# Performance work log

Measured on AMD Instinct MI355X. Metric: run time of the kernel, lower is better.

Reference implementation:

```python
import jax, jax.numpy as jnp
import numpy as np

N = 200000          # number of nodes (V)
NNZ = N * 32        # sparse adjacency non-zeros (avg degree 32)
D_IN, D_HID, N_CLASS = 128, 16, 40  # h = [nfeat, 2**(l+2), nclass] for l=2


def setup_inputs() -> dict:
    key = jax.random.key(0)
    ks = jax.random.split(key, 8)
    H = jax.random.normal(ks[0], (N, D_IN), dtype=jnp.float32)
    rows = jax.random.randint(ks[1], (NNZ,), 0, N)
    cols = jax.random.randint(ks[2], (NNZ,), 0, N)
    # symnormalised adjacency values are positive floats in (0,1]
    vals = jax.random.uniform(ks[3], (NNZ,), dtype=jnp.float32)
    std1 = 1.0 / np.sqrt(D_HID)
    W1 = jax.random.uniform(ks[4], (D_IN, D_HID), jnp.float32, -std1, std1)
    b1 = jax.random.uniform(ks[5], (D_HID,), jnp.float32, -std1, std1)
    std2 = 1.0 / np.sqrt(N_CLASS)
    W2 = jax.random.uniform(ks[6], (D_HID, N_CLASS), jnp.float32, -std2, std2)
    b2 = jax.random.uniform(ks[7], (N_CLASS,), jnp.float32, -std2, std2)
    return {"H": H, "rows": rows, "cols": cols, "vals": vals,
            "W1": W1, "b1": b1, "W2": W2, "b2": b2}


def spmm(rows, cols, vals, X):
    # Sparse [N,N] @ dense [N,d]: gather source rows, scale by edge weight,
    # scatter-add into destination rows (SparseMM.apply(A, HW)).
    gathered = X[cols] * vals[:, None]          # [nnz, d]
    return jax.ops.segment_sum(gathered, rows, num_segments=N)


def reference(H, rows, cols, vals, W1, b1, W2, b2):
    # layer 1: relu(A @ (H W1) + b1); dropout is identity in eval mode
    H1 = jax.nn.relu(spmm(rows, cols, vals, H @ W1) + b1)
    # layer 2: relu(A @ (H1 W2) + b2)
    H2 = jax.nn.relu(spmm(rows, cols, vals, H1 @ W2) + b2)
    return jax.nn.log_softmax(H2, axis=1)
```

## Files before the change

kernel.cpp:

```cpp
#include <hip/hip_runtime.h>

#define DIN   128
#define DHID  16
#define NCLS  40
#define RSH_C 9
#define RROWS_C 512
#define BATCH 8192
#define EPT   (BATCH/512)
#define CAPB  17920u

__device__ __forceinline__ unsigned short f2bf(float f) {
    unsigned u = __float_as_uint(f);
    unsigned r = (u + 0x7FFFu + ((u >> 16) & 1u)) >> 16;
    return (unsigned short)r;
}

__device__ __forceinline__ unsigned wave_iscan(unsigned x, int lane) {
#pragma unroll
    for (int off = 1; off < 64; off <<= 1) {
        unsigned t = __shfl_up(x, off, 64);
        if (lane >= off) x += t;
    }
    return x;
}

__global__ __launch_bounds__(256) void k1_gemm_lds(
    const float* __restrict__ H, const float* __restrict__ W1,
    unsigned short* __restrict__ X1, int n)
{
    __shared__ float ht[64 * 129];
    __shared__ __align__(16) float w[DIN * DHID];
    int tid = threadIdx.x;
    for (int i = tid; i < DIN * DHID; i += 256) w[i] = W1[i];
    int r0 = blockIdx.x * 64;
    int nr = n - r0; if (nr > 64) nr = 64;
    const float4* src = (const float4*)(H + (size_t)r0 * DIN);
    int n4 = nr * 32;
    for (int i4 = tid; i4 < n4; i4 += 256) {
        float4 v = src[i4];
        int row = i4 >> 5, c = (i4 & 31) << 2;
        float* d = &ht[row * 129 + c];
        d[0] = v.x; d[1] = v.y; d[2] = v.z; d[3] = v.w;
    }
    __syncthreads();
    int row = tid >> 2, q = tid & 3;
    if (row >= nr) return;
    const float* hrow = &ht[row * 129];
    const float* wq = &w[q * 4];
    float a0 = 0.f, a1 = 0.f, a2 = 0.f, a3 = 0.f;
#pragma unroll 8
    for (int k = 0; k < DIN; ++k) {
        float hk = hrow[k];
        float4 wv = *(const float4*)&wq[k * DHID];
        a0 += hk * wv.x; a1 += hk * wv.y; a2 += hk * wv.z; a3 += hk * wv.w;
    }
    uint2 pk;
    pk.x = (unsigned)f2bf(a0) | ((unsigned)f2bf(a1) << 16);
    pk.y = (unsigned)f2bf(a2) | ((unsigned)f2bf(a3) << 16);
    *(uint2*)(X1 + (size_t)(r0 + row) * DHID + q * 4) = pk;
}

__global__ __launch_bounds__(512) void k_init_cur(unsigned* __restrict__ cur_b, int nb)
{
    int i = threadIdx.x;
    if (i < nb) cur_b[i] = (unsigned)i * CAPB;
}

__global__ __launch_bounds__(512) void k_bucket2(
    const int* __restrict__ rows, const int* __restrict__ cols,
    const float* __restrict__ vals, unsigned* __restrict__ gcur,
    unsigned* __restrict__ colB, unsigned short* __restrict__ rowB,
    int nnz, int nb, int half)
{
    __shared__ unsigned stC[BATCH];
    __shared__ unsigned short stR[BATCH];
    __shared__ unsigned short bbk[BATCH];
    __shared__ unsigned hp[512];
    __shared__ unsigned short sstart[512];
    __shared__ unsigned gbase[512];
    __shared__ unsigned wsum[8];
    int tid = threadIdx.x;
    int e0 = blockIdx.x * BATCH;
    int m = nnz - e0; if (m > BATCH) m = BATCH;

    hp[tid] = 0;

    unsigned rec_[EPT]; unsigned bk_[EPT];
#pragma unroll
    for (int q = 0; q < EPT; ++q) {
        int i = q * 512 + tid;
        if (i < m) {
            int r = rows[e0 + i];
            int c = cols[e0 + i];
            float v = vals[e0 + i];
            unsigned qv = (unsigned)(v * 16383.f + 0.5f);
            if (qv > 16383u) qv = 16383u;
            rec_[q] = ((unsigned)c & 0x3FFFFu) | (qv << 18);
            unsigned key = (((unsigned)r & (RROWS_C - 1)) << 1) | (c >= half ? 1u : 0u);
            bk_[q] = (((unsigned)r >> RSH_C) << 10) | key;
        }
    }
    __syncthreads();
#pragma unroll
    for (int q = 0; q < EPT; ++q)
        if (q * 512 + tid < m) atomicAdd(&hp[bk_[q] >> 10], 1u);
    __syncthreads();
    unsigned v = hp[tid];
    unsigned gb = (tid < nb && v) ? atomicAdd(&gcur[tid], v) : 0u;
    int lane = tid & 63, wv = tid >> 6;
    unsigned x = wave_iscan(v, lane);
    if (lane == 63) wsum[wv] = x;
    gbase[tid] = gb;
    __syncthreads();
    unsigned wex = 0;
#pragma unroll
    for (int w = 0; w < 8; ++w) if (w < wv) wex += wsum[w];
    unsigned excl = x + wex - v;
    sstart[tid] = (unsigned short)excl;
    hp[tid] = excl;
    __syncthreads();
#pragma unroll
    for (int q = 0; q < EPT; ++q) {
        if (q * 512 + tid < m) {
            int b = bk_[q] >> 10;
            unsigned p = atomicAdd(&hp[b], 1u);
            stC[p] = rec_[q];
            stR[p] = (unsigned short)(bk_[q] & 1023u);
            bbk[p] = (unsigned short)b;
        }
    }
    __syncthreads();
    for (int i = tid; i < m; i += 512) {
        unsigned b = bbk[i];
        unsigned dst = gbase[b] + (i - (unsigned)sstart[b]);
        if (dst < (b + 1u) * CAPB) {
            colB[dst] = stC[i];
            rowB[dst] = stR[i];
        }
    }
}

__global__ __launch_bounds__(512) void k_sortb2(
    const unsigned* __restrict__ cur_b, unsigned* colB,
    const unsigned short* __restrict__ rowB,
    unsigned* __restrict__ rs4, int n, int nb)
{
    __shared__ unsigned st[CAPB];
    __shared__ unsigned c1[1024];
    __shared__ unsigned pos[1024];
    __shared__ unsigned wsum[8];
    int b = blockIdx.x, tid = threadIdx.x;
    unsigned s0 = (unsigned)b * CAPB;
    int m = (int)(cur_b[b] - s0);
    if (m > (int)CAPB) m = (int)CAPB;
    for (int i = tid; i < 1024; i += 512) c1[i] = 0;
    __syncthreads();
    for (int i = tid; i < m; i += 512)
        atomicAdd(&c1[rowB[s0 + i]], 1u);
    __syncthreads();
    unsigned c0 = c1[2 * tid], cA = c1[2 * tid + 1];
    unsigned p = c0 + cA;
    int lane = tid & 63, wvi = tid >> 6;
    unsigned x = wave_iscan(p, lane);
    if (lane == 63) wsum[wvi] = x;
    __syncthreads();
    unsigned wex = 0;
#pragma unroll
    for (int w = 0; w < 8; ++w) if (w < wvi) wex += wsum[w];
    unsigned excl = x + wex - p;
    pos[2 * tid] = excl;
    pos[2 * tid + 1] = excl + c0;
    int row = b * RROWS_C + tid;
    if (row < n) {
        uint4 rr;
        rr.x = s0 + excl;
        rr.y = s0 + excl + c0;
        rr.z = rr.y;
        rr.w = rr.y + cA;
        *(uint4*)(rs4 + ((size_t)row << 2)) = rr;
    }
    __syncthreads();
    for (int i = tid; i < m; i += 512) {
        unsigned q = atomicAdd(&pos[rowB[s0 + i]], 1u);
        st[q] = colB[s0 + i];
    }
    __syncthreads();
    for (int i = tid; i < m; i += 512)
        colB[s0 + i] = st[i];
}

template<int PASS, int FIN>
__global__ __launch_bounds__(256) void k_spmm16(
    const unsigned* __restrict__ rs4, const unsigned* __restrict__ colv2,
    const unsigned short* __restrict__ srcb,
    const float* __restrict__ bias,
    const float* __restrict__ W2,
    float* __restrict__ Ppart, unsigned short* __restrict__ dstb,
    float* __restrict__ out, int n)
{
    __shared__ float w2s[DHID * NCLS + NCLS];
    if (FIN == 3) {
        for (int i = threadIdx.x; i < DHID * NCLS; i += 256) w2s[i] = W2[i];
        if (threadIdx.x < NCLS) w2s[DHID * NCLS + threadIdx.x] = bias[threadIdx.x];
        __syncthreads();
    }
    const float DQ = 1.f / 16383.f;
    int row = blockIdx.x * 16 + (threadIdx.x >> 4);
    if (row >= n) return;
    int lane = threadIdx.x & 63;
    int sub = lane & 15;
    int g = sub >> 1, l = sub & 1;
    uint2 se = *(const uint2*)(rs4 + ((size_t)row << 2) + 2 * PASS);
    unsigned s0 = se.x, s1 = se.y;
    float a[8];
#pragma unroll
    for (int j = 0; j < 8; ++j) a[j] = 0.f;
    for (unsigned i = s0 + g; i < s1; i += 8) {
        unsigned rec = colv2[i];
        float vv = (float)(rec >> 18) * DQ;
        uint4 d = *((const uint4*)(srcb + (size_t)(rec & 0x3FFFFu) * DHID) + l);
        a[0] += __uint_as_float(d.x << 16) * vv;
        a[1] += __uint_as_float(d.x & 0xFFFF0000u) * vv;
        a[2] += __uint_as_float(d.y << 16) * vv;
        a[3] += __uint_as_float(d.y & 0xFFFF0000u) * vv;
        a[4] += __uint_as_float(d.z << 16) * vv;
        a[5] += __uint_as_float(d.z & 0xFFFF0000u) * vv;
        a[6] += __uint_as_float(d.w << 16) * vv;
        a[7] += __uint_as_float(d.w & 0xFFFF0000u) * vv;
    }
#pragma unroll
    for (int off = 2; off < 16; off <<= 1) {
#pragma unroll
        for (int j = 0; j < 8; ++j) a[j] += __shfl_xor(a[j], off, 64);
    }
    if (FIN == 0) {
        if (g == 0) {
            float* pp = Ppart + (size_t)row * DHID + l * 8;
            ((float4*)pp)[0] = make_float4(a[0], a[1], a[2], a[3]);
            ((float4*)pp)[1] = make_float4(a[4], a[5], a[6], a[7]);
        }
    } else if (FIN == 1) {
        if (g == 0) {
            const float* pp = Ppart + (size_t)row * DHID + l * 8;
            float4 p0 = ((const float4*)pp)[0], p1 = ((const float4*)pp)[1];
            a[0] += p0.x; a[1] += p0.y; a[2] += p0.z; a[3] += p0.w;
            a[4] += p1.x; a[5] += p1.y; a[6] += p1.z; a[7] += p1.w;
            float4 b0 = ((const float4*)(bias + l * 8))[0];
            float4 b1v = ((const float4*)(bias + l * 8))[1];
            float r0 = fmaxf(a[0] + b0.x, 0.f), r1 = fmaxf(a[1] + b0.y, 0.f);
            float r2 = fmaxf(a[2] + b0.z, 0.f), r3 = fmaxf(a[3] + b0.w, 0.f);
            float r4 = fmaxf(a[4] + b1v.x, 0.f), r5 = fmaxf(a[5] + b1v.y, 0.f);
            float r6 = fmaxf(a[6] + b1v.z, 0.f), r7 = fmaxf(a[7] + b1v.w, 0.f);
            uint4 pk;
            pk.x = (unsigned)f2bf(r0) | ((unsigned)f2bf(r1) << 16);
            pk.y = (unsigned)f2bf(r2) | ((unsigned)f2bf(r3) << 16);
            pk.z = (unsigned)f2bf(r4) | ((unsigned)f2bf(r5) << 16);
            pk.w = (unsigned)f2bf(r6) | ((unsigned)f2bf(r7) << 16);
            *(uint4*)(dstb + (size_t)row * DHID + l * 8) = pk;
        }
    } else {
        const float* pp = Ppart + (size_t)row * DHID + l * 8;
        float4 p0 = ((const float4*)pp)[0], p1 = ((const float4*)pp)[1];
        a[0] += p0.x; a[1] += p0.y; a[2] += p0.z; a[3] += p0.w;
        a[4] += p1.x; a[5] += p1.y; a[6] += p1.z; a[7] += p1.w;
        int base = lane & 48;
        float t[DHID];
#pragma unroll
        for (int k = 0; k < DHID; ++k)
            t[k] = __shfl(a[k & 7], base + (k >> 3), 64);
        float oc[3];
        float mx = 0.f;
#pragma unroll
        for (int q = 0; q < 3; ++q) {
            int c = sub + q * 16;
            float o = 0.f;
            if (c < NCLS) {
                o = w2s[DHID * NCLS + c];
#pragma unroll
                for (int k = 0; k < DHID; ++k) o += t[k] * w2s[k * NCLS + c];
                o = fmaxf(o, 0.f);
                mx = fmaxf(mx, o);
            }
            oc[q] = o;
        }
#pragma unroll
        for (int off = 1; off < 16; off <<= 1)
            mx = fmaxf(mx, __shfl_xor(mx, off, 64));
        float s = 0.f;
#pragma unroll
        for (int q = 0; q < 3; ++q) {
            int c = sub + q * 16;
            if (c < NCLS) s += __expf(oc[q] - mx);
        }
#pragma unroll
        for (int off = 1; off < 16; off <<= 1)
            s += __shfl_xor(s, off, 64);
        float ls = mx + __logf(s);
#pragma unroll
        for (int q = 0; q < 3; ++q) {
            int c = sub + q * 16;
            if (c < NCLS) out[(size_t)row * NCLS + c] = oc[q] - ls;
        }
    }
}

__global__ __launch_bounds__(256) void k4_final(
    const float* __restrict__ T, const float* __restrict__ W2,
    const float* __restrict__ b2, float* __restrict__ out, int n)
{
    __shared__ __align__(16) float w[DHID * NCLS];
    __shared__ float bb[NCLS];
    for (int i = threadIdx.x; i < DHID * NCLS; i += 256) w[i] = W2[i];
    if (threadIdx.x < NCLS) bb[threadIdx.x] = b2[threadIdx.x];
    __syncthreads();
    int r = blockIdx.x * 256 + threadIdx.x;
    if (r >= n) return;
    float t[DHID];
    const float4* trow = (const float4*)(T + (size_t)r * DHID);
#pragma unroll
    for (int q = 0; q < DHID / 4; ++q) {
        float4 v = trow[q];
        t[4*q+0] = v.x; t[4*q+1] = v.y; t[4*q+2] = v.z; t[4*q+3] = v.w;
    }
    float o[NCLS];
#pragma unroll
    for (int j = 0; j < NCLS; ++j) o[j] = bb[j];
#pragma unroll 4
    for (int k = 0; k < DHID; ++k) {
        float tk = t[k];
#pragma unroll
        for (int j4 = 0; j4 < NCLS / 4; ++j4) {
            float4 wv = *(const float4*)&w[k * NCLS + 4 * j4];
            o[4*j4+0] += tk * wv.x;
            o[4*j4+1] += tk * wv.y;
            o[4*j4+2] += tk * wv.z;
            o[4*j4+3] += tk * wv.w;
        }
    }
    float mx = 0.f;
#pragma unroll
    for (int j = 0; j < NCLS; ++j) {
        o[j] = fmaxf(o[j], 0.f);
        mx = fmaxf(mx, o[j]);
    }
    float s = 0.f;
#pragma unroll
    for (int j = 0; j < NCLS; ++j) s += __expf(o[j] - mx);
    float ls = mx + __logf(s);
    float4* orow = (float4*)(out + (size_t)r * NCLS);
#pragma unroll
    for (int j4 = 0; j4 < NCLS / 4; ++j4)
        orow[j4] = make_float4(o[4*j4+0]-ls, o[4*j4+1]-ls, o[4*j4+2]-ls, o[4*j4+3]-ls);
}

__global__ __launch_bounds__(256) void k1_gemm_hw1_f32(
    const float* __restrict__ H, const float* __restrict__ W1,
    float* __restrict__ X1, int n)
{
    __shared__ __align__(16) float w[DIN * DHID];
    for (int i = threadIdx.x; i < DIN * DHID; i += 256) w[i] = W1[i];
    __syncthreads();
    int r = blockIdx.x * 256 + threadIdx.x;
    if (r >= n) return;
    const float4* hrow = (const float4*)(H + (size_t)r * DIN);
    float acc[DHID];
#pragma unroll
    for (int j = 0; j < DHID; ++j) acc[j] = 0.f;
    for (int k4 = 0; k4 < DIN / 4; ++k4) {
        float4 h = hrow[k4];
        float hh[4] = {h.x, h.y, h.z, h.w};
#pragma unroll
        for (int kk = 0; kk < 4; ++kk)
#pragma unroll
            for (int j = 0; j < DHID; ++j)
                acc[j] += hh[kk] * w[(4 * k4 + kk) * DHID + j];
    }
    float4* o = (float4*)(X1 + (size_t)r * DHID);
#pragma unroll
    for (int q = 0; q < DHID / 4; ++q)
        o[q] = make_float4(acc[4*q], acc[4*q+1], acc[4*q+2], acc[4*q+3]);
}

__global__ __launch_bounds__(256) void k2_scatter16(
    const int* __restrict__ rows, const int* __restrict__ cols,
    const float* __restrict__ vals, const float* __restrict__ src,
    const float* __restrict__ bias, int do_relu,
    float* __restrict__ dst, int nnz)
{
    unsigned int tid = blockIdx.x * 256u + threadIdx.x;
    int e = (int)(tid >> 4);
    int j = (int)(tid & 15u);
    if (e >= nnz) return;
    int c = cols[e];
    int r = rows[e];
    float x = src[(size_t)c * DHID + j];
    if (do_relu) x = fmaxf(x + bias[j], 0.f);
    atomicAdd(&dst[(size_t)r * DHID + j], x * vals[e]);
}

extern "C" void kernel_launch(void* const* d_in, const int* in_sizes, int n_in,
                              void* d_out, int out_size, void* d_ws, size_t ws_size,
                              hipStream_t stream)
{
    const float* H    = (const float*)d_in[0];
    const int*   rows = (const int*)d_in[1];
    const int*   cols = (const int*)d_in[2];
    const float* vals = (const float*)d_in[3];
    const float* W1   = (const float*)d_in[4];
    const float* b1   = (const float*)d_in[5];
    const float* W2   = (const float*)d_in[6];
    const float* b2   = (const float*)d_in[7];
    float* out = (float*)d_out;

    int n   = in_sizes[0] / DIN;
    int nnz = in_sizes[1];
    int nb  = (n + RROWS_C - 1) >> RSH_C;
    int half = n >> 1;

    size_t off = 0;
    unsigned* cur_b = (unsigned*)d_ws;
    off = 512 * sizeof(unsigned);
    off = (off + 63) & ~(size_t)63;
    unsigned* rs4 = (unsigned*)((char*)d_ws + off);
    off += (size_t)4 * n * sizeof(unsigned);
    off = (off + 63) & ~(size_t)63;
    unsigned* colB = (unsigned*)((char*)d_ws + off);
    off += (size_t)nb * CAPB * sizeof(unsigned);
    off = (off + 63) & ~(size_t)63;
    unsigned short* rowB = (unsigned short*)((char*)d_ws + off);
    off += (size_t)nb * CAPB * sizeof(unsigned short);
    off = (off + 63) & ~(size_t)63;
    unsigned short* X1 = (unsigned short*)((char*)d_ws + off);
    off += (size_t)n * DHID * sizeof(unsigned short);
    off = (off + 63) & ~(size_t)63;
    unsigned short* H1 = (unsigned short*)((char*)d_ws + off);
    off += (size_t)n * DHID * sizeof(unsigned short);
    off = (off + 63) & ~(size_t)63;
    float* Ppart = (float*)((char*)d_ws + off);
    size_t needed = off + (size_t)n * DHID * sizeof(float);

    int rb = (n + 255) / 256;
    int sg = (n + 15) / 16;

    if (nb <= 512 && n <= (1 << 18) && needed <= ws_size) {
        k_init_cur<<<1, 512, 0, stream>>>(cur_b, nb);
        int nbk = (nnz + BATCH - 1) / BATCH;
        k_bucket2<<<nbk, 512, 0, stream>>>(rows, cols, vals, cur_b, colB, rowB, nnz, nb, half);
        k_sortb2<<<nb, 512, 0, stream>>>(cur_b, colB, rowB, rs4, n, nb);
        k1_gemm_lds<<<(n + 63) / 64, 256, 0, stream>>>(H, W1, X1, n);
        k_spmm16<0, 0><<<sg, 256, 0, stream>>>(rs4, colB, X1, nullptr, nullptr, Ppart, nullptr, nullptr, n);
        k_spmm16<1, 1><<<sg, 256, 0, stream>>>(rs4, colB, X1, b1, nullptr, Ppart, H1, nullptr, n);
        k_spmm16<0, 0><<<sg, 256, 0, stream>>>(rs4, colB, H1, nullptr, nullptr, Ppart, nullptr, nullptr, n);
        k_spmm16<1, 3><<<sg, 256, 0, stream>>>(rs4, colB, H1, b2, W2, Ppart, nullptr, out, n);
    } else {
        float* A = (float*)d_ws;
        float* B = A + (size_t)n * DHID;
        unsigned int sb = (unsigned int)(((long long)nnz * DHID + 255) / 256);
        k1_gemm_hw1_f32<<<rb, 256, 0, stream>>>(H, W1, A, n);
        hipMemsetAsync(B, 0, (size_t)n * DHID * sizeof(float), stream);
        k2_scatter16<<<sb, 256, 0, stream>>>(rows, cols, vals, A, nullptr, 0, B, nnz);
        hipMemsetAsync(A, 0, (size_t)n * DHID * sizeof(float), stream);
        k2_scatter16<<<sb, 256, 0, stream>>>(rows, cols, vals, B, b1, 1, A, nnz);
        k4_final<<<rb, 256, 0, stream>>>(A, W2, b2, out, n);
    }
}
```

Before: 270.4 us.

## Replace atomic global bucket cursors with per-batch counts and scanned offsets

The bucketing pass no longer reserves global slots with atomics into fixed-capacity buckets. Each batch now writes its locally sorted records contiguously and stores per-bucket counts and start offsets. Two small scan kernels compute bucket totals and prefix offsets, and the sort kernel gathers each bucket's segments from all batches. This gives a deterministic, compact layout without per-bucket capacity padding and lets the X1/H1/Ppart buffers alias the staging area. The cost is two extra launches and a sort pass whose inner loop reads about 782 short, scattered segments per bucket, one thread at a time.

New measurement: 370.1 us. +36.9%, slower.

```diff
diff --git a/kernel.cpp b/kernel.cpp
--- a/kernel.cpp
+++ b/kernel.cpp
@@ -8,6 +8,7 @@
 #define BATCH 8192
 #define EPT   (BATCH/512)
 #define CAPB  17920u
+#define NBKP  800
 
 __device__ __forceinline__ unsigned short f2bf(float f) {
     unsigned u = __float_as_uint(f);
@@ -60,24 +61,17 @@
     *(uint2*)(X1 + (size_t)(r0 + row) * DHID + q * 4) = pk;
 }
 
-__global__ __launch_bounds__(512) void k_init_cur(unsigned* __restrict__ cur_b, int nb)
-{
-    int i = threadIdx.x;
-    if (i < nb) cur_b[i] = (unsigned)i * CAPB;
-}
-
-__global__ __launch_bounds__(512) void k_bucket2(
+__global__ __launch_bounds__(512) void k_bucket3(
     const int* __restrict__ rows, const int* __restrict__ cols,
-    const float* __restrict__ vals, unsigned* __restrict__ gcur,
-    unsigned* __restrict__ colB, unsigned short* __restrict__ rowB,
+    const float* __restrict__ vals,
+    unsigned* __restrict__ colS, unsigned short* __restrict__ keyS,
+    unsigned short* __restrict__ CNT, unsigned short* __restrict__ SST,
     int nnz, int nb, int half)
 {
     __shared__ unsigned stC[BATCH];
-    __shared__ unsigned short stR[BATCH];
-    __shared__ unsigned short bbk[BATCH];
+    __shared__ unsigned short stK[BATCH];
     __shared__ unsigned hp[512];
     __shared__ unsigned short sstart[512];
-    __shared__ unsigned gbase[512];
     __shared__ unsigned wsum[8];
     int tid = threadIdx.x;
     int e0 = blockIdx.x * BATCH;
@@ -106,11 +100,9 @@
         if (q * 512 + tid < m) atomicAdd(&hp[bk_[q] >> 10], 1u);
     __syncthreads();
     unsigned v = hp[tid];
-    unsigned gb = (tid < nb && v) ? atomicAdd(&gcur[tid], v) : 0u;
     int lane = tid & 63, wv = tid >> 6;
     unsigned x = wave_iscan(v, lane);
     if (lane == 63) wsum[wv] = x;
-    gbase[tid] = gb;
     __syncthreads();
     unsigned wex = 0;
 #pragma unroll
@@ -118,6 +110,8 @@
     unsigned excl = x + wex - v;
     sstart[tid] = (unsigned short)excl;
     hp[tid] = excl;
+    CNT[(size_t)blockIdx.x * 512 + tid] = (unsigned short)v;
+    SST[(size_t)blockIdx.x * 512 + tid] = (unsigned short)excl;
     __syncthreads();
 #pragma unroll
     for (int q = 0; q < EPT; ++q) {
@@ -125,40 +119,82 @@
             int b = bk_[q] >> 10;
             unsigned p = atomicAdd(&hp[b], 1u);
             stC[p] = rec_[q];
-            stR[p] = (unsigned short)(bk_[q] & 1023u);
-            bbk[p] = (unsigned short)b;
+            stK[p] = (unsigned short)(bk_[q] & 1023u);
         }
     }
     __syncthreads();
     for (int i = tid; i < m; i += 512) {
-        unsigned b = bbk[i];
-        unsigned dst = gbase[b] + (i - (unsigned)sstart[b]);
-        if (dst < (b + 1u) * CAPB) {
-            colB[dst] = stC[i];
-            rowB[dst] = stR[i];
-        }
-    }
-}
-
-__global__ __launch_bounds__(512) void k_sortb2(
-    const unsigned* __restrict__ cur_b, unsigned* colB,
-    const unsigned short* __restrict__ rowB,
-    unsigned* __restrict__ rs4, int n, int nb)
+        colS[e0 + i] = stC[i];
+        keyS[e0 + i] = stK[i];
+    }
+}
+
+__global__ __launch_bounds__(512) void k_scanA(
+    const unsigned short* __restrict__ CNT, unsigned* __restrict__ tot, int nbk)
+{
+    __shared__ unsigned ws[8];
+    int b = blockIdx.x, tid = threadIdx.x;
+    unsigned s = 0;
+    for (int i = tid; i < nbk; i += 512) s += CNT[(size_t)i * 512 + b];
+#pragma unroll
+    for (int off = 1; off < 64; off <<= 1) s += __shfl_xor(s, off, 64);
+    if ((tid & 63) == 0) ws[tid >> 6] = s;
+    __syncthreads();
+    if (tid == 0) {
+        unsigned t2 = 0;
+#pragma unroll
+        for (int w = 0; w < 8; ++w) t2 += ws[w];
+        tot[b] = t2;
+    }
+}
+
+__global__ __launch_bounds__(512) void k_scanB(
+    const unsigned* __restrict__ tot, unsigned* __restrict__ RS, int nb)
+{
+    __shared__ unsigned wsum[8];
+    int tid = threadIdx.x;
+    unsigned v = (tid < nb) ? tot[tid] : 0u;
+    int lane = tid & 63, wv = tid >> 6;
+    unsigned x = wave_iscan(v, lane);
+    if (lane == 63) wsum[wv] = x;
+    __syncthreads();
+    unsigned wex = 0;
+#pragma unroll
+    for (int w = 0; w < 8; ++w) if (w < wv) wex += wsum[w];
+    if (tid < nb) RS[tid] = x + wex - v;
+    if (tid == nb - 1) RS[nb] = x + wex;
+}
+
+__global__ __launch_bounds__(512) void k_sortb3(
+    const unsigned* __restrict__ colS, const unsigned short* __restrict__ keyS,
+    const unsigned short* __restrict__ CNT, const unsigned short* __restrict__ SST,
+    const unsigned* __restrict__ RS,
+    unsigned* __restrict__ colB, unsigned* __restrict__ rs4,
+    int n, int nb, int nbk)
 {
     __shared__ unsigned st[CAPB];
-    __shared__ unsigned c1[1024];
-    __shared__ unsigned pos[1024];
+    __shared__ unsigned cp[1024];
+    __shared__ unsigned short CNTl[NBKP];
+    __shared__ unsigned short SSTl[NBKP];
     __shared__ unsigned wsum[8];
     int b = blockIdx.x, tid = threadIdx.x;
-    unsigned s0 = (unsigned)b * CAPB;
-    int m = (int)(cur_b[b] - s0);
-    if (m > (int)CAPB) m = (int)CAPB;
-    for (int i = tid; i < 1024; i += 512) c1[i] = 0;
-    __syncthreads();
-    for (int i = tid; i < m; i += 512)
-        atomicAdd(&c1[rowB[s0 + i]], 1u);
-    __syncthreads();
-    unsigned c0 = c1[2 * tid], cA = c1[2 * tid + 1];
+    for (int i = tid; i < nbk; i += 512) {
+        CNTl[i] = CNT[(size_t)i * 512 + b];
+        SSTl[i] = SST[(size_t)i * 512 + b];
+    }
+    for (int i = tid; i < 1024; i += 512) cp[i] = 0;
+    unsigned s0 = RS[b];
+    unsigned m = RS[b + 1] - s0;
+    if (m > CAPB) m = CAPB;
+    __syncthreads();
+    for (int i = tid; i < nbk; i += 512) {
+        unsigned c = CNTl[i];
+        size_t src = (size_t)i * BATCH + SSTl[i];
+        for (unsigned r = 0; r < c; ++r)
+            atomicAdd(&cp[keyS[src + r]], 1u);
+    }
+    __syncthreads();
+    unsigned c0 = cp[2 * tid], cA = cp[2 * tid + 1];
     unsigned p = c0 + cA;
     int lane = tid & 63, wvi = tid >> 6;
     unsigned x = wave_iscan(p, lane);
@@ -168,8 +204,8 @@
 #pragma unroll
     for (int w = 0; w < 8; ++w) if (w < wvi) wex += wsum[w];
     unsigned excl = x + wex - p;
-    pos[2 * tid] = excl;
-    pos[2 * tid + 1] = excl + c0;
+    cp[2 * tid] = excl;
+    cp[2 * tid + 1] = excl + c0;
     int row = b * RROWS_C + tid;
     if (row < n) {
         uint4 rr;
@@ -180,12 +216,16 @@
         *(uint4*)(rs4 + ((size_t)row << 2)) = rr;
     }
     __syncthreads();
-    for (int i = tid; i < m; i += 512) {
-        unsigned q = atomicAdd(&pos[rowB[s0 + i]], 1u);
-        st[q] = colB[s0 + i];
-    }
-    __syncthreads();
-    for (int i = tid; i < m; i += 512)
+    for (int i = tid; i < nbk; i += 512) {
+        unsigned c = CNTl[i];
+        size_t src = (size_t)i * BATCH + SSTl[i];
+        for (unsigned r = 0; r < c; ++r) {
+            unsigned q = atomicAdd(&cp[keyS[src + r]], 1u);
+            if (q < CAPB) st[q] = colS[src + r];
+        }
+    }
+    __syncthreads();
+    for (unsigned i = tid; i < m; i += 512)
         colB[s0 + i] = st[i];
 }
 
@@ -193,8 +233,7 @@
 __global__ __launch_bounds__(256) void k_spmm16(
     const unsigned* __restrict__ rs4, const unsigned* __restrict__ colv2,
     const unsigned short* __restrict__ srcb,
-    const float* __restrict__ bias,
-    const float* __restrict__ W2,
+    const float* __restrict__ bias, const float* __restrict__ W2,
     float* __restrict__ Ppart, unsigned short* __restrict__ dstb,
     float* __restrict__ out, int n)
 {
@@ -415,38 +454,45 @@
     int n   = in_sizes[0] / DIN;
     int nnz = in_sizes[1];
     int nb  = (n + RROWS_C - 1) >> RSH_C;
+    int nbk = (nnz + BATCH - 1) / BATCH;
     int half = n >> 1;
 
     size_t off = 0;
-    unsigned* cur_b = (unsigned*)d_ws;
-    off = 512 * sizeof(unsigned);
+    unsigned* tot = (unsigned*)d_ws;
+    unsigned* RS  = tot + 512;
+    off = (512 + 513) * sizeof(unsigned);
     off = (off + 63) & ~(size_t)63;
     unsigned* rs4 = (unsigned*)((char*)d_ws + off);
     off += (size_t)4 * n * sizeof(unsigned);
     off = (off + 63) & ~(size_t)63;
+    unsigned short* CNT = (unsigned short*)((char*)d_ws + off);
+    off += (size_t)NBKP * 512 * sizeof(unsigned short);
+    unsigned short* SST = (unsigned short*)((char*)d_ws + off);
+    off += (size_t)NBKP * 512 * sizeof(unsigned short);
+    off = (off + 63) & ~(size_t)63;
     unsigned* colB = (unsigned*)((char*)d_ws + off);
-    off += (size_t)nb * CAPB * sizeof(unsigned);
+    off += (size_t)nnz * sizeof(unsigned);
     off = (off + 63) & ~(size_t)63;
-    unsigned short* rowB = (unsigned short*)((char*)d_ws + off);
-    off += (size_t)nb * CAPB * sizeof(unsigned short);
+    size_t offS = off;
+    unsigned* colS = (unsigned*)((char*)d_ws + off);
+    size_t regS = (size_t)nnz * sizeof(unsigned);
+    size_t regT = (size_t)n * DHID * (2 + 2 + 4);
+    off += (regS > regT ? regS : regT);
     off = (off + 63) & ~(size_t)63;
-    unsigned short* X1 = (unsigned short*)((char*)d_ws + off);
-    off += (size_t)n * DHID * sizeof(unsigned short);
-    off = (off + 63) & ~(size_t)63;
-    unsigned short* H1 = (unsigned short*)((char*)d_ws + off);
-    off += (size_t)n * DHID * sizeof(unsigned short);
-    off = (off + 63) & ~(size_t)63;
-    float* Ppart = (float*)((char*)d_ws + off);
-    size_t needed = off + (size_t)n * DHID * sizeof(float);
+    unsigned short* keyS = (unsigned short*)((char*)d_ws + off);
+    size_t needed = off + (size_t)nnz * sizeof(unsigned short);
+    unsigned short* X1 = (unsigned short*)((char*)d_ws + offS);
+    unsigned short* H1 = X1 + (size_t)n * DHID;
+    float* Ppart = (float*)(H1 + (size_t)n * DHID);
 
     int rb = (n + 255) / 256;
     int sg = (n + 15) / 16;
 
-    if (nb <= 512 && n <= (1 << 18) && needed <= ws_size) {
-        k_init_cur<<<1, 512, 0, stream>>>(cur_b, nb);
-        int nbk = (nnz + BATCH - 1) / BATCH;
-        k_bucket2<<<nbk, 512, 0, stream>>>(rows, cols, vals, cur_b, colB, rowB, nnz, nb, half);
-        k_sortb2<<<nb, 512, 0, stream>>>(cur_b, colB, rowB, rs4, n, nb);
+    if (nb <= 512 && nbk <= NBKP && n <= (1 << 18) && needed <= ws_size) {
+        k_bucket3<<<nbk, 512, 0, stream>>>(rows, cols, vals, colS, keyS, CNT, SST, nnz, nb, half);
+        k_scanA<<<nb, 512, 0, stream>>>(CNT, tot, nbk);
+        k_scanB<<<1, 512, 0, stream>>>(tot, RS, nb);
+        k_sortb3<<<nb, 512, 0, stream>>>(colS, keyS, CNT, SST, RS, colB, rs4, n, nb, nbk);
         k1_gemm_lds<<<(n + 63) / 64, 256, 0, stream>>>(H, W1, X1, n);
         k_spmm16<0, 0><<<sg, 256, 0, stream>>>(rs4, colB, X1, nullptr, nullptr, Ppart, nullptr, nullptr, n);
         k_spmm16<1, 1><<<sg, 256, 0, stream>>>(rs4, colB, X1, b1, nullptr, Ppart, H1, nullptr, n);
```
